# Optimization experiments

Measured on AMD Instinct MI355X. Metric: run time of the kernel, lower is better.

## Reference

```python
import jax, jax.numpy as jnp
import numpy as np

THRESHOLD = 0.7


def ternary_dequant(w, threshold=THRESHOLD):
    """Ternary quantize {-1,0,+1} with masked-mean alpha, return ternary*alpha."""
    abs_w = jnp.abs(w)
    delta = threshold * jnp.mean(abs_w)
    ternary = jnp.where(w > delta, 1.0, jnp.where(w < -delta, -1.0, 0.0)).astype(w.dtype)
    nz = ternary != 0
    cnt = jnp.sum(nz)
    # alpha = mean(|w| over nonzero ternary entries); fall back to mean(|w|) if all-zero
    masked_sum = jnp.sum(jnp.where(nz, abs_w, 0.0))
    alpha = jnp.where(cnt > 0, masked_sum / jnp.maximum(cnt, 1).astype(w.dtype), jnp.mean(abs_w))
    return ternary * alpha


def setup_inputs() -> dict:
    key = jax.random.key(0)
    kx, kw, kb = jax.random.split(key, 3)
    B, S, D_IN, D_OUT = 4, 2048, 4096, 4096
    x = jax.random.normal(kx, (B * S, D_IN), dtype=jnp.float32)
    # xavier-uniform-ish init for latent FP32 weights
    limit = np.sqrt(6.0 / (D_IN + D_OUT)).astype(np.float32)
    weight = jax.random.uniform(kw, (D_OUT, D_IN), dtype=jnp.float32, minval=-limit, maxval=limit)
    bias = jax.random.normal(kb, (D_OUT,), dtype=jnp.float32) * 0.02
    return {"x": x, "weight": weight, "bias": bias}


def reference(x, weight, bias):
    q_weight = ternary_dequant(weight)  # (out, in)
    return jnp.matmul(x, q_weight.T) + bias  # (tokens, out)
```

## Files before the change

### kernel.cpp

```cpp
#include <hip/hip_runtime.h>

#define M_DIM 8192
#define N_DIM 4096
#define K_DIM 4096

typedef __attribute__((ext_vector_type(8))) __bf16 bf16x8;
typedef __attribute__((ext_vector_type(4))) __bf16 bf16x4;
typedef __attribute__((ext_vector_type(4))) float floatx4;

__device__ __forceinline__ void async_copy16(const void* g, void* l) {
    __builtin_amdgcn_global_load_lds(
        (const __attribute__((address_space(1))) void*)g,
        (__attribute__((address_space(3))) void*)l,
        16, 0, 0);
}

__device__ __forceinline__ void block_sync() {
    asm volatile("" ::: "memory");
    __builtin_amdgcn_s_barrier();
    asm volatile("" ::: "memory");
}

__device__ __forceinline__ double wave_reduce_d(double v) {
    #pragma unroll
    for (int o = 32; o > 0; o >>= 1) v += __shfl_down(v, o, 64);
    return v;
}
__device__ __forceinline__ unsigned wave_reduce_u(unsigned v) {
    #pragma unroll
    for (int o = 32; o > 0; o >>= 1) v += __shfl_down(v, o, 64);
    return v;
}

__global__ __launch_bounds__(256) void k_pre(const float4* __restrict__ w4,
                                             double* __restrict__ part,
                                             const float4* __restrict__ x4,
                                             bf16x4* __restrict__ xb) {
    const int tid = threadIdx.x;
    if (blockIdx.x < 2048) {
        int idx = blockIdx.x * 256 + tid;
        double s = 0.0;
        #pragma unroll
        for (int it = 0; it < 8; ++it) {
            float4 v = w4[idx + it * (2048 * 256)];
            s += (double)fabsf(v.x) + (double)fabsf(v.y) +
                 (double)fabsf(v.z) + (double)fabsf(v.w);
        }
        s = wave_reduce_d(s);
        __shared__ double sm[4];
        if ((tid & 63) == 0) sm[tid >> 6] = s;
        __syncthreads();
        if (tid == 0) part[blockIdx.x] = sm[0] + sm[1] + sm[2] + sm[3];
    } else {
        int idx = (blockIdx.x - 2048) * 256 + tid;
        #pragma unroll
        for (int it = 0; it < 4; ++it) {
            int i = idx + it * (8192 * 256);
            float4 v = x4[i];
            bf16x4 o;
            o[0] = (__bf16)v.x; o[1] = (__bf16)v.y;
            o[2] = (__bf16)v.z; o[3] = (__bf16)v.w;
            xb[i] = o;
        }
    }
}

__global__ __launch_bounds__(256) void k_quant(const float4* __restrict__ w4,
                                               bf16x4* __restrict__ tern,
                                               const double* __restrict__ part,
                                               double* __restrict__ scal,
                                               double* __restrict__ pm,
                                               unsigned* __restrict__ pc) {
    const int tid = threadIdx.x;
    double s = 0.0;
    #pragma unroll
    for (int i = 0; i < 8; ++i) s += part[tid + i * 256];
    s = wave_reduce_d(s);
    __shared__ double sm[4];
    if ((tid & 63) == 0) sm[tid >> 6] = s;
    __syncthreads();
    const double mean = (sm[0] + sm[1] + sm[2] + sm[3]) * (1.0 / 16777216.0);
    const double delta = 0.7 * mean;
    if (blockIdx.x == 0 && tid == 0) scal[0] = mean;

    int idx = blockIdx.x * 256 + tid;
    double msum = 0.0;
    unsigned cnt = 0;
    #pragma unroll
    for (int it = 0; it < 8; ++it) {
        int i = idx + it * (2048 * 256);
        float4 v = w4[i];
        float e[4] = {v.x, v.y, v.z, v.w};
        bf16x4 o;
        #pragma unroll
        for (int c = 0; c < 4; ++c) {
            float wv = e[c];
            float t = ((double)wv > delta) ? 1.0f
                    : (((double)wv < -delta) ? -1.0f : 0.0f);
            if (t != 0.0f) { msum += (double)fabsf(wv); cnt++; }
            o[c] = (__bf16)t;
        }
        tern[i] = o;
    }
    msum = wave_reduce_d(msum);
    cnt  = wave_reduce_u(cnt);
    __shared__ double smd[4];
    __shared__ unsigned smu[4];
    if ((tid & 63) == 0) { smd[tid >> 6] = msum; smu[tid >> 6] = cnt; }
    __syncthreads();
    if (tid == 0) {
        pm[blockIdx.x] = smd[0] + smd[1] + smd[2] + smd[3];
        pc[blockIdx.x] = smu[0] + smu[1] + smu[2] + smu[3];
    }
}

__global__ __launch_bounds__(512, 2) void ternary_gemm(
    const __bf16* __restrict__ A,
    const __bf16* __restrict__ B,
    const float*  __restrict__ bias,
    const double* __restrict__ scal,
    const double* __restrict__ pm,
    const unsigned* __restrict__ pc,
    float* __restrict__ C)
{
    __shared__ __attribute__((aligned(128))) __bf16 As[4][8192];
    __shared__ __attribute__((aligned(128))) __bf16 Bs[4][8192];
    __shared__ double smd[8];
    __shared__ unsigned smu[8];

    const int tid  = threadIdx.x;
    const int w    = tid >> 6;
    const int lane = tid & 63;
    const int quad = lane >> 4;
    const int l16  = lane & 15;
    const int wr = w >> 2;
    const int wc = w & 3;

    const int id = (blockIdx.x & 7) * 64 + (blockIdx.x >> 3);
    const int br = id >> 4;
    const int bc = id & 15;

    const int srow = lane >> 2;
    const int scol = ((lane & 3) ^ ((srow >> 1) & 3)) * 8;

    const __bf16* gA0 = A + (size_t)(br * 256 + w * 16 + srow) * K_DIM + scol;
    const __bf16* gA1 = gA0 + (size_t)128 * K_DIM;
    const __bf16* gB0 = B + (size_t)(bc * 256 + w * 16 + srow) * K_DIM + scol;
    const __bf16* gB1 = gB0 + (size_t)128 * K_DIM;

    floatx4 acc[8][4] = {};

    const int swz   = (quad ^ ((l16 >> 1) & 3)) * 8;
    const int a_off = (wr * 128 + l16) * 32 + swz;
    const int b_off = (wc * 64 + l16) * 32 + swz;

#define STAGE_A(ktt) do {                                        \
        const int _sb = (ktt) & 3; const int _so = (ktt) * 32;   \
        async_copy16(gA0 + _so, &As[_sb][w * 512]);              \
        async_copy16(gA1 + _so, &As[_sb][(w + 8) * 512]);        \
    } while (0)
#define STAGE_B(ktt) do {                                        \
        const int _sb = (ktt) & 3; const int _so = (ktt) * 32;   \
        async_copy16(gB0 + _so, &Bs[_sb][w * 512]);              \
        async_copy16(gB1 + _so, &Bs[_sb][(w + 8) * 512]);        \
    } while (0)

    STAGE_A(0); STAGE_B(0);
    STAGE_A(1); STAGE_B(1);
    STAGE_A(2); STAGE_B(2);

#define TILE(kt_, VMN, DO_STAGE_) do {                                         \
        asm volatile("s_waitcnt vmcnt(" #VMN ")" ::: "memory");                \
        block_sync();                                                          \
        const int _buf = (kt_) & 3;                                            \
        const __bf16* _Ab = As[_buf];                                          \
        const __bf16* _Bb = Bs[_buf];                                          \
        bf16x8 _a[4], _b[4];                                                   \
        _Pragma("unroll")                                                      \
        for (int i = 0; i < 4; ++i)                                            \
            _a[i] = *(const bf16x8*)(_Ab + a_off + i * 512);                   \
        _Pragma("unroll")                                                      \
        for (int j = 0; j < 4; ++j)                                            \
            _b[j] = *(const bf16x8*)(_Bb + b_off + j * 512);                   \
        if (DO_STAGE_) STAGE_A((kt_) + 3);                                     \
        block_sync();                                                          \
        __builtin_amdgcn_sched_barrier(0);                                     \
        __builtin_amdgcn_s_setprio(1);                                         \
        _Pragma("unroll")                                                      \
        for (int i = 0; i < 4; ++i)                                            \
            _Pragma("unroll")                                                  \
            for (int j = 0; j < 4; ++j)                                        \
                acc[i][j] = __builtin_amdgcn_mfma_f32_16x16x32_bf16(           \
                    _a[i], _b[j], acc[i][j], 0, 0, 0);                         \
        __builtin_amdgcn_s_setprio(0);                                         \
        __builtin_amdgcn_sched_barrier(0);                                     \
        block_sync();                                                          \
        _Pragma("unroll")                                                      \
        for (int i = 0; i < 4; ++i)                                            \
            _a[i] = *(const bf16x8*)(_Ab + a_off + (4 + i) * 512);             \
        if (DO_STAGE_) STAGE_B((kt_) + 3);                                     \
        block_sync();                                                          \
        __builtin_amdgcn_sched_barrier(0);                                     \
        __builtin_amdgcn_s_setprio(1);                                         \
        _Pragma("unroll")                                                      \
        for (int i = 0; i < 4; ++i)                                            \
            _Pragma("unroll")                                                  \
            for (int j = 0; j < 4; ++j)                                        \
                acc[4 + i][j] = __builtin_amdgcn_mfma_f32_16x16x32_bf16(       \
                    _a[i], _b[j], acc[4 + i][j], 0, 0, 0);                     \
        __builtin_amdgcn_s_setprio(0);                                         \
        __builtin_amdgcn_sched_barrier(0);                                     \
    } while (0)

    for (int kt = 0; kt < 125; ++kt) TILE(kt, 8, true);
    TILE(125, 8, false);
    TILE(126, 4, false);
    TILE(127, 0, false);

#undef TILE
#undef STAGE_A
#undef STAGE_B

    double s = 0.0; unsigned c = 0;
    #pragma unroll
    for (int i = 0; i < 4; ++i) { s += pm[tid + i * 512]; c += pc[tid + i * 512]; }
    s = wave_reduce_d(s);
    c = wave_reduce_u(c);
    if (lane == 0) { smd[w] = s; smu[w] = c; }
    __syncthreads();
    double ms = 0.0; unsigned ct = 0;
    #pragma unroll
    for (int i = 0; i < 8; ++i) { ms += smd[i]; ct += smu[i]; }
    const float alpha = (float)(ct > 0 ? ms / (double)ct : scal[0]);

    float bv[4];
    #pragma unroll
    for (int j = 0; j < 4; ++j)
        bv[j] = bias[bc * 256 + wc * 64 + j * 16 + l16];

    #pragma unroll
    for (int i = 0; i < 8; ++i) {
        const int row0 = br * 256 + wr * 128 + i * 16 + quad * 4;
        #pragma unroll
        for (int j = 0; j < 4; ++j) {
            const int col = bc * 256 + wc * 64 + j * 16 + l16;
            #pragma unroll
            for (int r = 0; r < 4; ++r)
                C[(size_t)(row0 + r) * N_DIM + col] = acc[i][j][r] * alpha + bv[j];
        }
    }
}

extern "C" void kernel_launch(void* const* d_in, const int* in_sizes, int n_in,
                              void* d_out, int out_size, void* d_ws, size_t ws_size,
                              hipStream_t stream) {
    const float* x    = (const float*)d_in[0];
    const float* w    = (const float*)d_in[1];
    const float* bias = (const float*)d_in[2];
    float* out = (float*)d_out;

    char* ws = (char*)d_ws;
    double*   d_scal = (double*)ws;
    double*   part   = (double*)(ws + 64);
    double*   pm     = (double*)(ws + 16448);
    unsigned* pc     = (unsigned*)(ws + 32832);
    __bf16*   xb     = (__bf16*)(ws + 65536);
    __bf16*   tern   = (__bf16*)(ws + 65536 + (size_t)M_DIM * K_DIM * 2);

    k_pre<<<10240, 256, 0, stream>>>((const float4*)w, part, (const float4*)x, (bf16x4*)xb);
    k_quant<<<2048, 256, 0, stream>>>((const float4*)w, (bf16x4*)tern, part, d_scal, pm, pc);

    ternary_gemm<<<512, 512, 0, stream>>>(xb, tern, bias, d_scal, pm, pc, out);
}
```

Measured before the change: 602.3 us.

## Use one barrier per k-tile with inline-asm LDS reads and manual waitcnts

Restructures the GEMM main loop so each k-tile has a single s_barrier instead of four. All eight A fragments and four B fragments are read from LDS up front using inline ds_read_b128 with precomputed LDS addresses. Both async global-to-LDS stage copies are issued together, and explicit lgkmcnt waits gate the two MFMA halves. The aim is to cut barrier stalls and let LDS reads overlap with MFMA work. In exchange, more registers are live, and correctness depends on the hand-written waitcnt placement, because the compiler cannot track the inline-asm loads.

```diff
diff --git a/kernel.cpp b/kernel.cpp
--- a/kernel.cpp
+++ b/kernel.cpp
@@ -15,10 +15,13 @@
         16, 0, 0);
 }
 
-__device__ __forceinline__ void block_sync() {
-    asm volatile("" ::: "memory");
-    __builtin_amdgcn_s_barrier();
-    asm volatile("" ::: "memory");
+__device__ __forceinline__ unsigned lds_addr(const void* p) {
+    return (unsigned)(unsigned long long)(const __attribute__((address_space(3))) void*)p;
+}
+__device__ __forceinline__ bf16x8 lds_read_b128(unsigned addr) {
+    bf16x8 r;
+    asm volatile("ds_read_b128 %0, %1" : "=v"(r) : "v"(addr));
+    return r;
 }
 
 __device__ __forceinline__ double wave_reduce_d(double v) {
@@ -154,6 +157,9 @@
     const int a_off = (wr * 128 + l16) * 32 + swz;
     const int b_off = (wc * 64 + l16) * 32 + swz;
 
+    const unsigned aAddr0 = lds_addr(&As[0][0]) + (unsigned)(a_off * 2);
+    const unsigned bAddr0 = lds_addr(&Bs[0][0]) + (unsigned)(b_off * 2);
+
 #define STAGE_A(ktt) do {                                        \
         const int _sb = (ktt) & 3; const int _so = (ktt) * 32;   \
         async_copy16(gA0 + _so, &As[_sb][w * 512]);              \
@@ -171,19 +177,20 @@
 
 #define TILE(kt_, VMN, DO_STAGE_) do {                                         \
         asm volatile("s_waitcnt vmcnt(" #VMN ")" ::: "memory");                \
-        block_sync();                                                          \
-        const int _buf = (kt_) & 3;                                            \
-        const __bf16* _Ab = As[_buf];                                          \
-        const __bf16* _Bb = Bs[_buf];                                          \
-        bf16x8 _a[4], _b[4];                                                   \
+        __builtin_amdgcn_s_barrier();                                          \
+        const unsigned _bufB = (unsigned)(((kt_) & 3) * 16384);                \
+        bf16x8 _a[8], _b[4];                                                   \
         _Pragma("unroll")                                                      \
         for (int i = 0; i < 4; ++i)                                            \
-            _a[i] = *(const bf16x8*)(_Ab + a_off + i * 512);                   \
+            _a[i] = lds_read_b128(aAddr0 + _bufB + (unsigned)(i * 1024));      \
         _Pragma("unroll")                                                      \
         for (int j = 0; j < 4; ++j)                                            \
-            _b[j] = *(const bf16x8*)(_Bb + b_off + j * 512);                   \
-        if (DO_STAGE_) STAGE_A((kt_) + 3);                                     \
-        block_sync();                                                          \
+            _b[j] = lds_read_b128(bAddr0 + _bufB + (unsigned)(j * 1024));      \
+        _Pragma("unroll")                                                      \
+        for (int i = 4; i < 8; ++i)                                            \
+            _a[i] = lds_read_b128(aAddr0 + _bufB + (unsigned)(i * 1024));      \
+        if (DO_STAGE_) { STAGE_A((kt_) + 3); STAGE_B((kt_) + 3); }             \
+        asm volatile("s_waitcnt lgkmcnt(4)" ::: "memory");                     \
         __builtin_amdgcn_sched_barrier(0);                                     \
         __builtin_amdgcn_s_setprio(1);                                         \
         _Pragma("unroll")                                                      \
@@ -193,13 +200,7 @@
                 acc[i][j] = __builtin_amdgcn_mfma_f32_16x16x32_bf16(           \
                     _a[i], _b[j], acc[i][j], 0, 0, 0);                         \
         __builtin_amdgcn_s_setprio(0);                                         \
-        __builtin_amdgcn_sched_barrier(0);                                     \
-        block_sync();                                                          \
-        _Pragma("unroll")                                                      \
-        for (int i = 0; i < 4; ++i)                                            \
-            _a[i] = *(const bf16x8*)(_Ab + a_off + (4 + i) * 512);             \
-        if (DO_STAGE_) STAGE_B((kt_) + 3);                                     \
-        block_sync();                                                          \
+        asm volatile("s_waitcnt lgkmcnt(0)" ::: "memory");                     \
         __builtin_amdgcn_sched_barrier(0);                                     \
         __builtin_amdgcn_s_setprio(1);                                         \
         _Pragma("unroll")                                                      \
@@ -207,7 +208,7 @@
             _Pragma("unroll")                                                  \
             for (int j = 0; j < 4; ++j)                                        \
                 acc[4 + i][j] = __builtin_amdgcn_mfma_f32_16x16x32_bf16(       \
-                    _a[i], _b[j], acc[4 + i][j], 0, 0, 0);                     \
+                    _a[4 + i], _b[j], acc[4 + i][j], 0, 0, 0);                 \
         __builtin_amdgcn_s_setprio(0);                                         \
         __builtin_amdgcn_sched_barrier(0);                                     \
     } while (0)
@@ -270,5 +271,6 @@
     k_pre<<<10240, 256, 0, stream>>>((const float4*)w, part, (const float4*)x, (bf16x4*)xb);
     k_quant<<<2048, 256, 0, stream>>>((const float4*)w, (bf16x4*)tern, part, d_scal, pm, pc);
 
-    ternary_gemm<<<512, 512, 0, stream>>>(xb, tern, bias, d_scal, pm, pc, out);
-}
+    dim3 grid(512);
+    ternary_gemm<<<grid, 512, 0, stream>>>(xb, tern, bias, d_scal, pm, pc, out);
+}
```

Measured after the change: 516.3 us. 14.3% less time.
